# Kernel optimization log

Hardware: AMD Instinct MI355X
Metric: run time of the kernel (lower is better)

## Reference

```python
import jax, jax.numpy as jnp
import numpy as np

N_NODES = 200000
N_EDGES = 3200000
N_FEAT = 128
N_GRAPHS = 1000
N_CLASSES = 10
K = 30          # sort-pool k
C_CAT = 97      # 32+32+32+1 concatenated channels


def _glorot(k, shape):
    fan = shape[0] + shape[-1]
    return jax.random.normal(k, shape, jnp.float32) * (2.0 / fan) ** 0.5


def setup_inputs() -> dict:
    key = jax.random.key(0)
    ks = jax.random.split(key, 20)
    x = jax.random.normal(ks[0], (N_NODES, N_FEAT), jnp.float32)
    edge_index = jax.random.randint(ks[1], (2, N_EDGES), 0, N_NODES, jnp.int32)
    batch = jnp.sort(jax.random.randint(ks[2], (N_NODES,), 0, N_GRAPHS, jnp.int32))
    params = dict(
        W1=_glorot(ks[3], (N_FEAT, 32)), b1=jnp.zeros((32,), jnp.float32),
        W2=_glorot(ks[4], (32, 32)),     b2=jnp.zeros((32,), jnp.float32),
        W3=_glorot(ks[5], (32, 32)),     b3=jnp.zeros((32,), jnp.float32),
        W4=_glorot(ks[6], (32, 1)),      b4=jnp.zeros((1,), jnp.float32),
        conv5_w=_glorot(ks[7], (16, 1, 97)),  conv5_b=jnp.zeros((16,), jnp.float32),
        conv6_w=_glorot(ks[8], (32, 16, 5)),  conv6_b=jnp.zeros((32,), jnp.float32),
        fc1_w=_glorot(ks[9], (352, 128)),     fc1_b=jnp.zeros((128,), jnp.float32),
        fc2_w=_glorot(ks[10], (128, N_CLASSES)), fc2_b=jnp.zeros((N_CLASSES,), jnp.float32),
    )
    return dict(x=x, edge_index=edge_index, batch=batch, **params)


def reference(x, edge_index, batch, W1, b1, W2, b2, W3, b3, W4, b4,
              conv5_w, conv5_b, conv6_w, conv6_b, fc1_w, fc1_b, fc2_w, fc2_b):
    N = x.shape[0]
    src, dst = edge_index[0], edge_index[1]
    emask = (src != dst).astype(x.dtype)            # remove_self_loops
    deg = jax.ops.segment_sum(emask, dst, num_segments=N) + 1.0  # +1 for added self-loop
    inv_sqrt = jax.lax.rsqrt(deg)
    coef = emask * inv_sqrt[src] * inv_sqrt[dst]    # D^-1/2 (A) D^-1/2 edge weight
    inv_deg = 1.0 / deg                             # self-loop weight

    def gcn(h, W, b):
        hw = h @ W
        agg = jax.ops.segment_sum(hw[src] * coef[:, None], dst, num_segments=N)
        return agg + hw * inv_deg[:, None] + b

    x1 = jnp.tanh(gcn(x, W1, b1))
    x2 = jnp.tanh(gcn(x1, W2, b2))
    x3 = jnp.tanh(gcn(x2, W3, b3))
    x4 = jnp.tanh(gcn(x3, W4, b4))
    xc = jnp.concatenate([x1, x2, x3, x4], axis=-1)  # [N, 97]

    # SortAggregation(k=30): per-graph descending sort by last channel, top-k, zero pad
    perm = jnp.lexsort((-xc[:, -1], batch))          # batch-major, last channel desc
    xs, bs = xc[perm], batch[perm]
    counts = jax.ops.segment_sum(jnp.ones_like(batch), batch, num_segments=N_GRAPHS)
    starts = jnp.cumsum(counts) - counts
    rank = jnp.arange(N, dtype=jnp.int32) - starts[bs]
    valid = rank < K
    pooled = jnp.zeros((N_GRAPHS, K, C_CAT), xc.dtype).at[
        bs, jnp.where(valid, rank, K - 1)].add(jnp.where(valid[:, None], xs, 0.0))

    z = pooled.reshape(N_GRAPHS, 1, K * C_CAT)       # [G, 1, 2910]
    dn = ('NCH', 'OIH', 'NCH')
    z = jax.lax.conv_general_dilated(z, conv5_w, (97,), 'VALID', dimension_numbers=dn)
    z = jax.nn.relu(z + conv5_b[None, :, None])      # [G, 16, 30]
    z = jax.lax.reduce_window(z, -jnp.inf, jax.lax.max, (1, 1, 2), (1, 1, 2), 'VALID')
    z = jax.lax.conv_general_dilated(z, conv6_w, (1,), 'VALID', dimension_numbers=dn)
    z = jax.nn.relu(z + conv6_b[None, :, None])      # [G, 32, 11]
    z = z.reshape(N_GRAPHS, -1)                      # [G, 352]
    h = jax.nn.relu(z @ fc1_w + fc1_b)               # dropout is identity in eval
    return jax.nn.log_softmax(h @ fc2_w + fc2_b, axis=-1)
```

## Files before the change

kernel.cpp:

```cpp
#include <hip/hip_runtime.h>
#include <math.h>

#define NN 200000
#define NE 3200000
#define NF 128
#define NG 1000
#define KSEL 30
#define CCAT 97
#define EPADCAP (NE + 8 * NN)

#define BWID 512
#define NB 391
#define BCAP 10240
#define P1_CHUNK 8192
#define P1_BLKS 391
#define GCUR 400

__global__ void k_p1_partition(const int* __restrict__ ei, int* __restrict__ bcursor,
                               int* __restrict__ ebuf) {
    __shared__ int lhist[NB];
    __shared__ int lbase[NB];
    int tid = threadIdx.x;
    int base = blockIdx.x * P1_CHUNK;
    for (int b = tid; b < NB; b += 256) lhist[b] = 0;
    __syncthreads();
    for (int it = 0; it < P1_CHUNK / 256; it++) {
        int e = base + it * 256 + tid;
        if (e < NE) {
            int s = ei[e], d = ei[NE + e];
            if (s != d) atomicAdd(&lhist[d >> 9], 1);
        }
    }
    __syncthreads();
    for (int b = tid; b < NB; b += 256) {
        int cnt = lhist[b];
        lbase[b] = cnt ? atomicAdd(&bcursor[b], cnt) : 0;
        lhist[b] = 0;
    }
    __syncthreads();
    for (int it = 0; it < P1_CHUNK / 256; it++) {
        int e = base + it * 256 + tid;
        if (e < NE) {
            int s = ei[e], d = ei[NE + e];
            if (s != d) {
                int b = d >> 9;
                int r = atomicAdd(&lhist[b], 1);
                int pos = lbase[b] + r;
                if (pos >= BCAP) pos = BCAP - 1;
                ebuf[b * BCAP + pos] = s | ((d & 511) << 18);
            }
        }
    }
}

__global__ void k_p2_count(const int* __restrict__ bcursor, const int* __restrict__ ebuf,
                           int* __restrict__ rowstart, int* __restrict__ rowcnt8,
                           float* __restrict__ inv_sqrt, int* __restrict__ gcursor,
                           float* __restrict__ hwsA, float* __restrict__ hwsB) {
    __shared__ int lcnt[BWID];
    __shared__ int ps[256];
    __shared__ int sbase;
    int b = blockIdx.x;
    int tid = threadIdx.x;
    if (b == 0 && tid < 32) {
        hwsA[(size_t)NN * 32 + tid] = 0.0f;
        hwsB[(size_t)NN * 32 + tid] = 0.0f;
    }
    for (int i = tid; i < BWID; i += 256) lcnt[i] = 0;
    __syncthreads();
    int size = bcursor[b];
    if (size > BCAP) size = BCAP;
    const int* eb = ebuf + b * BCAP;
    for (int k = tid; k < size; k += 256) atomicAdd(&lcnt[eb[k] >> 18], 1);
    __syncthreads();
    int node0 = b * BWID;
    int i0 = 2 * tid, i1 = 2 * tid + 1;
    int c0raw = lcnt[i0], c1raw = lcnt[i1];
    int c0 = (node0 + i0 < NN) ? ((c0raw + 7) & ~7) : 0;
    int c1 = (node0 + i1 < NN) ? ((c1raw + 7) & ~7) : 0;
    int pair = c0 + c1;
    ps[tid] = pair;
    __syncthreads();
    for (int off = 1; off < 256; off <<= 1) {
        int a = (tid >= off) ? ps[tid - off] : 0;
        int cur = ps[tid];
        __syncthreads();
        ps[tid] = cur + a;
        __syncthreads();
    }
    if (tid == 255) sbase = atomicAdd(gcursor, ps[255]);
    int excl = ps[tid] - pair;
    __syncthreads();
    int rs0 = sbase + excl;
    int rs1 = rs0 + c0;
    int n0 = node0 + i0, n1 = node0 + i1;
    if (n0 < NN) {
        rowstart[n0] = rs0;
        rowcnt8[n0] = c0;
        inv_sqrt[n0] = rsqrtf((float)(c0raw + 1));
    }
    if (n1 < NN) {
        rowstart[n1] = rs1;
        rowcnt8[n1] = c1;
        inv_sqrt[n1] = rsqrtf((float)(c1raw + 1));
    }
}

__global__ void k_p3_scatter(const int* __restrict__ bcursor, const int* __restrict__ ebuf,
                             const int* __restrict__ rowstart, const int* __restrict__ rowcnt8,
                             int* __restrict__ esrc) {
    __shared__ int lcur[BWID];
    int b = blockIdx.x;
    int tid = threadIdx.x;
    int node0 = b * BWID;
    for (int i = tid; i < BWID; i += 256)
        lcur[i] = (node0 + i < NN) ? rowstart[node0 + i] : 0;
    __syncthreads();
    int size = bcursor[b];
    if (size > BCAP) size = BCAP;
    const int* eb = ebuf + b * BCAP;
    for (int k = tid; k < size; k += 256) {
        int v = eb[k];
        int local = v >> 18;
        int pos = atomicAdd(&lcur[local], 1);
        esrc[pos] = v & 0x3FFFF;
    }
    __syncthreads();
    for (int i = tid; i < BWID; i += 256) {
        int node = node0 + i;
        if (node < NN) {
            int end = rowstart[node] + rowcnt8[node];
            for (int p = lcur[i]; p < end; p++) esrc[p] = NN;
        }
    }
}

template <int K>
__global__ void __launch_bounds__(256, 3) k_mm(const float* __restrict__ X,
                                               const float* __restrict__ W,
                                               const float* __restrict__ inv_sqrt,
                                               float* __restrict__ Y) {
    constexpr int K4 = K / 4;
    constexpr int RS = K4 + 1;
    __shared__ float4 sW[K * 8];
    __shared__ float4 sX[64 * RS];
    int tid = threadIdx.x;
    for (int i = tid; i < K * 8; i += 256) sW[i] = ((const float4*)W)[i];
    const float4* __restrict__ Xg = (const float4*)(X + (size_t)blockIdx.x * 64 * K);
    for (int i = tid; i < 64 * K4; i += 256) {
        int row = i / K4;
        int col = i & (K4 - 1);
        sX[row * RS + col] = Xg[i];
    }
    __syncthreads();
    int g = tid >> 3;
    int q = tid & 7;
    int r0 = blockIdx.x * 64 + g * 2;
    const float4* __restrict__ xr0 = &sX[(size_t)(g * 2 + 0) * RS];
    const float4* __restrict__ xr1 = &sX[(size_t)(g * 2 + 1) * RS];
    float4 a0 = make_float4(0.f, 0.f, 0.f, 0.f);
    float4 a1 = make_float4(0.f, 0.f, 0.f, 0.f);
#pragma unroll 4
    for (int k4 = 0; k4 < K4; k4++) {
        float4 x0 = xr0[k4];
        float4 x1 = xr1[k4];
        const float4* wk = &sW[k4 * 32 + q];
#pragma unroll
        for (int kk = 0; kk < 4; kk++) {
            float4 w = wk[kk * 8];
            float s0 = (kk == 0) ? x0.x : (kk == 1) ? x0.y : (kk == 2) ? x0.z : x0.w;
            float s1 = (kk == 0) ? x1.x : (kk == 1) ? x1.y : (kk == 2) ? x1.z : x1.w;
            a0.x = fmaf(s0, w.x, a0.x); a0.y = fmaf(s0, w.y, a0.y);
            a0.z = fmaf(s0, w.z, a0.z); a0.w = fmaf(s0, w.w, a0.w);
            a1.x = fmaf(s1, w.x, a1.x); a1.y = fmaf(s1, w.y, a1.y);
            a1.z = fmaf(s1, w.z, a1.z); a1.w = fmaf(s1, w.w, a1.w);
        }
    }
    float s0 = inv_sqrt[r0 + 0];
    float s1 = inv_sqrt[r0 + 1];
    a0.x *= s0; a0.y *= s0; a0.z *= s0; a0.w *= s0;
    a1.x *= s1; a1.y *= s1; a1.z *= s1; a1.w *= s1;
    ((float4*)(Y + (size_t)(r0 + 0) * 32))[q] = a0;
    ((float4*)(Y + (size_t)(r0 + 1) * 32))[q] = a1;
}

template <int MODE>
__global__ void k_aggr_f(const int* __restrict__ rowstart, const int* __restrict__ rowcnt8,
                         const int* __restrict__ esrc,
                         const float* __restrict__ hws, const float* __restrict__ inv_sqrt,
                         const float* __restrict__ bvec, const float* __restrict__ Wn,
                         float* __restrict__ xout, float* __restrict__ hnext) {
    __shared__ float sxr[8][32];
    int t = blockIdx.x * 256 + threadIdx.x;
    int n = t >> 5, c = t & 31;
    int e0 = rowstart[n], e1 = e0 + rowcnt8[n];
    float a[8];
    a[0] = hws[(size_t)n * 32 + c];
#pragma unroll
    for (int k = 1; k < 8; k++) a[k] = 0.0f;
    for (int e = e0; e < e1; e += 8) {
        int4 sA = *(const int4*)(esrc + e);
        int4 sB = *(const int4*)(esrc + e + 4);
        float v0 = hws[(size_t)sA.x * 32 + c];
        float v1 = hws[(size_t)sA.y * 32 + c];
        float v2 = hws[(size_t)sA.z * 32 + c];
        float v3 = hws[(size_t)sA.w * 32 + c];
        float v4 = hws[(size_t)sB.x * 32 + c];
        float v5 = hws[(size_t)sB.y * 32 + c];
        float v6 = hws[(size_t)sB.z * 32 + c];
        float v7 = hws[(size_t)sB.w * 32 + c];
        a[0] += v0; a[1] += v1; a[2] += v2; a[3] += v3;
        a[4] += v4; a[5] += v5; a[6] += v6; a[7] += v7;
    }
    float acc = ((a[0] + a[1]) + (a[2] + a[3])) + ((a[4] + a[5]) + (a[6] + a[7]));
    float invs = inv_sqrt[n];
    float r = tanhf(fmaf(acc, invs, bvec[c]));
    xout[t] = r;
    if (MODE == 1) {
        int ln = threadIdx.x >> 5;
        sxr[ln][c] = r;
        float wcol[32];
#pragma unroll
        for (int k = 0; k < 32; k++) wcol[k] = Wn[k * 32 + c];
        __syncthreads();
        const float4* xr = (const float4*)sxr[ln];
        float h = 0.f;
#pragma unroll
        for (int j = 0; j < 8; j++) {
            float4 xq = xr[j];
            h = fmaf(xq.x, wcol[4 * j + 0], h);
            h = fmaf(xq.y, wcol[4 * j + 1], h);
            h = fmaf(xq.z, wcol[4 * j + 2], h);
            h = fmaf(xq.w, wcol[4 * j + 3], h);
        }
        hnext[t] = h * invs;
    } else {
        float v = r * Wn[c];
        v += __shfl_xor(v, 1);
        v += __shfl_xor(v, 2);
        v += __shfl_xor(v, 4);
        v += __shfl_xor(v, 8);
        v += __shfl_xor(v, 16);
        if (c == 0) hnext[n] = v * invs;
        if (t == 0) hnext[NN] = 0.f;
    }
}

__global__ void k_aggr1(const int* __restrict__ rowstart, const int* __restrict__ rowcnt8,
                        const int* __restrict__ esrc,
                        const float* __restrict__ hws4, const float* __restrict__ inv_sqrt,
                        const float* __restrict__ b4, float* __restrict__ x4) {
    int n = blockIdx.x * 256 + threadIdx.x;
    if (n >= NN) return;
    int e0 = rowstart[n], e1 = e0 + rowcnt8[n];
    float a[8];
    a[0] = hws4[n];
#pragma unroll
    for (int k = 1; k < 8; k++) a[k] = 0.0f;
    for (int e = e0; e < e1; e += 8) {
        int4 sA = *(const int4*)(esrc + e);
        int4 sB = *(const int4*)(esrc + e + 4);
        a[0] += hws4[sA.x]; a[1] += hws4[sA.y];
        a[2] += hws4[sA.z]; a[3] += hws4[sA.w];
        a[4] += hws4[sB.x]; a[5] += hws4[sB.y];
        a[6] += hws4[sB.z]; a[7] += hws4[sB.w];
    }
    float acc = ((a[0] + a[1]) + (a[2] + a[3])) + ((a[4] + a[5]) + (a[6] + a[7]));
    x4[n] = tanhf(fmaf(acc, inv_sqrt[n], b4[0]));
}

__global__ void k_gbounds(const int* __restrict__ batch, int* __restrict__ starts) {
    int n = blockIdx.x * 256 + threadIdx.x;
    if (n >= NN) return;
    int bn = batch[n];
    int bp = (n == 0) ? -1 : batch[n - 1];
    for (int g = bp + 1; g <= bn; g++) starts[g] = n;
    if (n == NN - 1)
        for (int g = bn + 1; g <= NG; g++) starts[g] = NN;
}

__global__ void k_tail(const int* __restrict__ starts,
                       const float* __restrict__ x1, const float* __restrict__ x2,
                       const float* __restrict__ x3, const float* __restrict__ x4,
                       const float* __restrict__ w5, const float* __restrict__ b5,
                       const float* __restrict__ w6, const float* __restrict__ b6,
                       const float* __restrict__ fw1, const float* __restrict__ fb1,
                       const float* __restrict__ fw2, const float* __restrict__ fb2,
                       float* __restrict__ out) {
    __shared__ float keys[1024];
    __shared__ int sel[KSEL];
    __shared__ float sP[KSEL * CCAT];
    __shared__ float s5[16 * 30];
    __shared__ float smp[16 * 15];
    __shared__ float sz[352];
    __shared__ float sh[128];
    __shared__ float sl[10];
    int g = blockIdx.x;
    int tid = threadIdx.x;
    int start = starts[g];
    int cnt = starts[g + 1] - start;
    if (cnt > 1024) cnt = 1024;
    for (int i = tid; i < cnt; i += 256) keys[i] = x4[start + i];
    __syncthreads();
    for (int i = tid; i < cnt; i += 256) {
        float ki = keys[i];
        int rank = 0;
        for (int j = 0; j < cnt; j++) {
            float kj = keys[j];
            rank += (kj > ki) || (kj == ki && j < i);
        }
        if (rank < KSEL) sel[rank] = start + i;
    }
    __syncthreads();
    int selcnt = cnt < KSEL ? cnt : KSEL;
    for (int t = tid; t < KSEL * CCAT; t += 256) {
        int r = t / CCAT, ch = t - r * CCAT;
        float v = 0.0f;
        if (r < selcnt) {
            int node = sel[r];
            if (ch < 32)      v = x1[(size_t)node * 32 + ch];
            else if (ch < 64) v = x2[(size_t)node * 32 + ch - 32];
            else if (ch < 96) v = x3[(size_t)node * 32 + ch - 64];
            else              v = x4[node];
        }
        sP[t] = v;
    }
    __syncthreads();
    for (int t = tid; t < 16 * 30; t += 256) {
        int c = t / 30, j = t - c * 30;
        float acc = b5[c];
        for (int i = 0; i < CCAT; i++) acc = fmaf(sP[j * CCAT + i], w5[c * CCAT + i], acc);
        s5[c * 30 + j] = fmaxf(acc, 0.0f);
    }
    __syncthreads();
    for (int t = tid; t < 16 * 15; t += 256) {
        int c = t / 15, j = t - c * 15;
        smp[t] = fmaxf(s5[c * 30 + 2 * j], s5[c * 30 + 2 * j + 1]);
    }
    __syncthreads();
    for (int t = tid; t < 32 * 11; t += 256) {
        int c = t / 11, j = t - c * 11;
        float acc = b6[c];
        for (int ci = 0; ci < 16; ci++) {
#pragma unroll
            for (int k = 0; k < 5; k++)
                acc = fmaf(smp[ci * 15 + j + k], w6[(c * 16 + ci) * 5 + k], acc);
        }
        sz[t] = fmaxf(acc, 0.0f);
    }
    __syncthreads();
    if (tid < 128) {
        float acc = fb1[tid];
        for (int i = 0; i < 352; i++) acc = fmaf(sz[i], fw1[i * 128 + tid], acc);
        sh[tid] = fmaxf(acc, 0.0f);
    }
    __syncthreads();
    if (tid < 10) {
        float acc = fb2[tid];
        for (int i = 0; i < 128; i++) acc = fmaf(sh[i], fw2[i * 10 + tid], acc);
        sl[tid] = acc;
    }
    __syncthreads();
    if (tid < 10) {
        float m = -1e30f;
        for (int i = 0; i < 10; i++) m = fmaxf(m, sl[i]);
        float ssum = 0.0f;
        for (int i = 0; i < 10; i++) ssum += expf(sl[i] - m);
        out[g * 10 + tid] = sl[tid] - m - logf(ssum);
    }
}

extern "C" void kernel_launch(void* const* d_in, const int* in_sizes, int n_in,
                              void* d_out, int out_size, void* d_ws, size_t ws_size,
                              hipStream_t stream) {
    const float* x   = (const float*)d_in[0];
    const int*   ei  = (const int*)d_in[1];
    const int*   bat = (const int*)d_in[2];
    const float* W1  = (const float*)d_in[3];
    const float* b1  = (const float*)d_in[4];
    const float* W2  = (const float*)d_in[5];
    const float* b2  = (const float*)d_in[6];
    const float* W3  = (const float*)d_in[7];
    const float* b3  = (const float*)d_in[8];
    const float* W4  = (const float*)d_in[9];
    const float* b4  = (const float*)d_in[10];
    const float* w5  = (const float*)d_in[11];
    const float* b5  = (const float*)d_in[12];
    const float* w6  = (const float*)d_in[13];
    const float* b6  = (const float*)d_in[14];
    const float* fw1 = (const float*)d_in[15];
    const float* fb1 = (const float*)d_in[16];
    const float* fw2 = (const float*)d_in[17];
    const float* fb2 = (const float*)d_in[18];
    float* out = (float*)d_out;

    float* ws = (float*)d_ws;
    float* inv_sqrt = ws;
    float* hwsA     = inv_sqrt + NN;
    float* hwsB     = hwsA + (size_t)(NN + 1) * 32;
    float* x1       = hwsB + (size_t)(NN + 1) * 32;
    float* x2       = x1 + (size_t)NN * 32;
    float* x3       = x2 + (size_t)NN * 32;
    float* x4       = x3 + (size_t)NN * 32;
    int* rowstart   = (int*)(x4 + NN);
    int* rowcnt8    = rowstart + NN;
    int* esrc       = rowcnt8 + NN;
    int* bcursor    = esrc + EPADCAP;
    int* gstarts    = bcursor + 512;
    int* ebuf       = (int*)x3;

    const int TB = 256;
    int gN  = (NN + TB - 1) / TB;
    int gNC = (NN * 32) / TB;
    int gMM = NN / 64;

    hipMemsetAsync(bcursor, 0, 512 * sizeof(int), stream);
    k_p1_partition<<<P1_BLKS, TB, 0, stream>>>(ei, bcursor, ebuf);
    k_p2_count<<<NB, TB, 0, stream>>>(bcursor, ebuf, rowstart, rowcnt8, inv_sqrt,
                                      bcursor + GCUR, hwsA, hwsB);
    k_p3_scatter<<<NB, TB, 0, stream>>>(bcursor, ebuf, rowstart, rowcnt8, esrc);

    k_gbounds<<<gN, TB, 0, stream>>>(bat, gstarts);

    k_mm<128><<<gMM, TB, 0, stream>>>(x, W1, inv_sqrt, hwsA);
    k_aggr_f<1><<<gNC, TB, 0, stream>>>(rowstart, rowcnt8, esrc, hwsA, inv_sqrt, b1, W2, x1, hwsB);
    k_aggr_f<1><<<gNC, TB, 0, stream>>>(rowstart, rowcnt8, esrc, hwsB, inv_sqrt, b2, W3, x2, hwsA);
    k_aggr_f<2><<<gNC, TB, 0, stream>>>(rowstart, rowcnt8, esrc, hwsA, inv_sqrt, b3, W4, x3, hwsB);
    k_aggr1<<<gN, TB, 0, stream>>>(rowstart, rowcnt8, esrc, hwsB, inv_sqrt, b4, x4);

    k_tail<<<NG, TB, 0, stream>>>(gstarts, x1, x2, x3, x4,
                                  w5, b5, w6, b6, fw1, fb1, fw2, fb2, out);
}
```

Baseline: 570.2 us.

## Order CSR rows by bucket via prefix scan and fold cursor zeroing into gbounds

Replaces the per-block atomic cursor that assigned CSR row-start offsets in arbitrary block order with a single-block exclusive scan over bucket sizes, plus fixed padding per bucket. Edge storage then follows node order, so aggregation reads the edge list more sequentially. The memset of the bucket cursors is removed and its zeroing moved into the k_gbounds kernel, which now runs first. This adds one small kernel launch. It relies on the per-bucket padding BPAD being enough to cover the round-up of row counts to multiples of 8.

```diff
diff --git a/kernel.cpp b/kernel.cpp
--- a/kernel.cpp
+++ b/kernel.cpp
@@ -14,7 +14,7 @@
 #define BCAP 10240
 #define P1_CHUNK 8192
 #define P1_BLKS 391
-#define GCUR 400
+#define BPAD 3584
 
 __global__ void k_p1_partition(const int* __restrict__ ei, int* __restrict__ bcursor,
                                int* __restrict__ ebuf) {
@@ -53,13 +53,29 @@
     }
 }
 
+__global__ void k_sb(const int* __restrict__ bcursor, int* __restrict__ bbase) {
+    __shared__ int s[512];
+    int tid = threadIdx.x;
+    int v = (tid < NB) ? bcursor[tid] : 0;
+    s[tid] = v;
+    __syncthreads();
+    for (int off = 1; off < 512; off <<= 1) {
+        int a = (tid >= off) ? s[tid - off] : 0;
+        int cur = s[tid];
+        __syncthreads();
+        s[tid] = cur + a;
+        __syncthreads();
+    }
+    if (tid < NB) bbase[tid] = s[tid] - v + tid * BPAD;
+}
+
 __global__ void k_p2_count(const int* __restrict__ bcursor, const int* __restrict__ ebuf,
+                           const int* __restrict__ bbase,
                            int* __restrict__ rowstart, int* __restrict__ rowcnt8,
-                           float* __restrict__ inv_sqrt, int* __restrict__ gcursor,
+                           float* __restrict__ inv_sqrt,
                            float* __restrict__ hwsA, float* __restrict__ hwsB) {
     __shared__ int lcnt[BWID];
     __shared__ int ps[256];
-    __shared__ int sbase;
     int b = blockIdx.x;
     int tid = threadIdx.x;
     if (b == 0 && tid < 32) {
@@ -88,10 +104,8 @@
         ps[tid] = cur + a;
         __syncthreads();
     }
-    if (tid == 255) sbase = atomicAdd(gcursor, ps[255]);
     int excl = ps[tid] - pair;
-    __syncthreads();
-    int rs0 = sbase + excl;
+    int rs0 = bbase[b] + excl;
     int rs1 = rs0 + c0;
     int n0 = node0 + i0, n1 = node0 + i1;
     if (n0 < NN) {
@@ -269,8 +283,14 @@
     x4[n] = tanhf(fmaf(acc, inv_sqrt[n], b4[0]));
 }
 
-__global__ void k_gbounds(const int* __restrict__ batch, int* __restrict__ starts) {
-    int n = blockIdx.x * 256 + threadIdx.x;
+__global__ void k_gbounds(const int* __restrict__ batch, int* __restrict__ starts,
+                          int* __restrict__ bcursor) {
+    int tid = threadIdx.x;
+    if (blockIdx.x == 0) {
+        bcursor[tid] = 0;
+        bcursor[256 + tid] = 0;
+    }
+    int n = blockIdx.x * 256 + tid;
     if (n >= NN) return;
     int bn = batch[n];
     int bp = (n == 0) ? -1 : batch[n - 1];
@@ -406,7 +426,8 @@
     int* rowcnt8    = rowstart + NN;
     int* esrc       = rowcnt8 + NN;
     int* bcursor    = esrc + EPADCAP;
-    int* gstarts    = bcursor + 512;
+    int* bbase      = bcursor + 512;
+    int* gstarts    = bbase + 512;
     int* ebuf       = (int*)x3;
 
     const int TB = 256;
@@ -414,13 +435,13 @@
     int gNC = (NN * 32) / TB;
     int gMM = NN / 64;
 
-    hipMemsetAsync(bcursor, 0, 512 * sizeof(int), stream);
+    k_gbounds<<<gN, TB, 0, stream>>>(bat, gstarts, bcursor);
+
     k_p1_partition<<<P1_BLKS, TB, 0, stream>>>(ei, bcursor, ebuf);
-    k_p2_count<<<NB, TB, 0, stream>>>(bcursor, ebuf, rowstart, rowcnt8, inv_sqrt,
-                                      bcursor + GCUR, hwsA, hwsB);
+    k_sb<<<1, 512, 0, stream>>>(bcursor, bbase);
+    k_p2_count<<<NB, TB, 0, stream>>>(bcursor, ebuf, bbase, rowstart, rowcnt8,
+                                      inv_sqrt, hwsA, hwsB);
     k_p3_scatter<<<NB, TB, 0, stream>>>(bcursor, ebuf, rowstart, rowcnt8, esrc);
-
-    k_gbounds<<<gN, TB, 0, stream>>>(bat, gstarts);
 
     k_mm<128><<<gMM, TB, 0, stream>>>(x, W1, inv_sqrt, hwsA);
     k_aggr_f<1><<<gNC, TB, 0, stream>>>(rowstart, rowcnt8, esrc, hwsA, inv_sqrt, b1, W2, x1, hwsB);
```

New measurement: 570.0 us. About the same (-0.0%).
